# Performance work log

Hardware: AMD Instinct MI355X
Metric: run time of the kernel (lower is better)

The kernel has to match this reference:

```python
import jax, jax.numpy as jnp
import numpy as np

L, B, H, R = 128, 4, 768, 24
LN_EPS = 1e-5


def setup_inputs() -> dict:
    key = jax.random.key(0)
    ks = jax.random.split(key, 10)
    s = 1.0 / np.sqrt(H)
    return {
        "h_re": jax.random.normal(ks[0], (L, B, H), jnp.float32),
        "h_share": jax.random.normal(ks[1], (L, B, H), jnp.float32),
        "mask": jnp.ones((L, B), jnp.float32),
        # r: Linear(2H -> H)
        "r_w": jax.random.normal(ks[2], (H, 2 * H), jnp.float32) * s,
        "r_b": jnp.zeros((H,), jnp.float32),
        # hid2hid: Linear(3H -> H)
        "hid_w": jax.random.normal(ks[3], (H, 3 * H), jnp.float32) * s,
        "hid_b": jnp.zeros((H,), jnp.float32),
        # LayerNorm(H)
        "ln_g": jnp.ones((H,), jnp.float32),
        "ln_b": jnp.zeros((H,), jnp.float32),
        # hid2rel: Linear(H -> R)
        "rel_w": jax.random.normal(ks[4], (R, H), jnp.float32) * s,
        "rel_b": jnp.zeros((R,), jnp.float32),
    }


def reference(h_re, h_share, mask, r_w, r_b, hid_w, hid_b, ln_g, ln_b, rel_w, rel_b):
    # h_global = max_over_length( tanh( Linear([h_share; h_re]) ) )  -> [B, H]
    # Decompose concat-linear into two additive projections (same math).
    w_sh, w_re = r_w[:, :H], r_w[:, H:]
    g = jnp.tanh(jnp.einsum('lbh,kh->lbk', h_share, w_sh)
                 + jnp.einsum('lbh,kh->lbk', h_re, w_re) + r_b)
    g = jnp.max(g, axis=0)  # [B, H]

    # hid2hid(cat(r1, r2, g)) = h_re@W1^T (bcast over j) + h_re@W2^T (bcast over i) + g@W3^T + b
    w1, w2, w3 = hid_w[:, :H], hid_w[:, H:2 * H], hid_w[:, 2 * H:]
    p1 = jnp.einsum('lbh,kh->lbk', h_re, w1)        # [L, B, H] -> varies with i
    p2 = jnp.einsum('lbh,kh->lbk', h_re, w2)        # [L, B, H] -> varies with j
    pg = jnp.einsum('bh,kh->bk', g, w3) + hid_b     # [B, H]
    z = p1[:, None, :, :] + p2[None, :, :, :] + pg  # [L, L, B, H]

    # LayerNorm over last dim
    mu = jnp.mean(z, axis=-1, keepdims=True)
    var = jnp.mean(jnp.square(z - mu), axis=-1, keepdims=True)
    z = (z - mu) * jax.lax.rsqrt(var + LN_EPS) * ln_g + ln_b

    # ELU (dropout = identity in eval), then sigmoid(hid2rel)
    z = jax.nn.elu(z)
    re = jax.nn.sigmoid(jnp.einsum('ijbh,rh->ijbr', z, rel_w) + rel_b)  # [L, L, B, R]

    # pairwise mask: mask[i,b] * mask[j,b]
    m = mask[:, None, :] * mask[None, :, :]        # [L, L, B]
    return re * m[..., None]
```

## Files before the change

kernel.cpp:

```cpp
#include <hip/hip_runtime.h>
#include <hip/hip_bf16.h>
#include <math.h>

#define L 128
#define B 4
#define H 768
#define LN_EPS 1e-5f
#define XROWS 272
#define DSTRIDE 73984

typedef __attribute__((ext_vector_type(8))) short short8;
typedef __attribute__((ext_vector_type(4))) float f32x4;
typedef __attribute__((ext_vector_type(16))) float f32x16;

static __device__ __forceinline__ unsigned f2bfu(float f) {
    unsigned u = __float_as_uint(f);
    return (u + 0x7FFFu + ((u >> 16) & 1u)) >> 16;
}
static __device__ __forceinline__ uint2 pk4(float4 v) {
    uint2 o;
    o.x = f2bfu(v.x) | (f2bfu(v.y) << 16);
    o.y = f2bfu(v.z) | (f2bfu(v.w) << 16);
    return o;
}
static __device__ __forceinline__ unsigned short f2b(float f) {
    union { __hip_bfloat16 h; unsigned short u; } cv;
    cv.h = __float2bfloat16(f);
    return cv.u;
}
static __device__ __forceinline__ float4 unpk4(uint2 p) {
    return make_float4(__uint_as_float(p.x << 16),
                       __uint_as_float(p.x & 0xffff0000u),
                       __uint_as_float(p.y << 16),
                       __uint_as_float(p.y & 0xffff0000u));
}
static __device__ __forceinline__ unsigned fkey(float x) {
    unsigned u = __float_as_uint(x);
    return (u >> 31) ? ~u : (u | 0x80000000u);
}

__global__ __launch_bounds__(256) void kConv(const float* __restrict__ h_re,
                                             const float* __restrict__ h_share,
                                             const float* __restrict__ r_w,
                                             const float* __restrict__ hid_w,
                                             const float* __restrict__ rel_w,
                                             unsigned short* __restrict__ apack,
                                             unsigned short* __restrict__ wpackA,
                                             unsigned short* __restrict__ wpackB,
                                             unsigned short* __restrict__ rwb2,
                                             unsigned int* __restrict__ gmax) {
    int t = blockIdx.x * 256 + threadIdx.x;
    if (t >= 397056) return;
    if (t < 98304) {
        int m = t / 192, oct = t % 192, k = oct * 8;
        const float* src = (k < 768) ? (h_share + (size_t)m * 768 + k)
                                     : (h_re + (size_t)m * 768 + k - 768);
        float4 x = *(const float4*)src, y = *(const float4*)(src + 4);
        int mt = m >> 4, lr = m & 15, ks = k >> 5, lq = (k >> 3) & 3;
        uint2* dst = (uint2*)(apack + (((size_t)mt * 48 + ks) * 64 + lq * 16 + lr) * 8);
        dst[0] = pk4(x); dst[1] = pk4(y);
    } else if (t < 245760) {
        int t2 = t - 98304;
        int n = t2 / 192, oct = t2 % 192, k = oct * 8;
        const float* src = r_w + (size_t)n * 1536 + k;
        float4 x = *(const float4*)src, y = *(const float4*)(src + 4);
        int nt = n >> 4, lr = n & 15, ks = k >> 5, lq = (k >> 3) & 3;
        uint2* dst = (uint2*)(wpackA + (((size_t)nt * 48 + ks) * 64 + lq * 16 + lr) * 8);
        dst[0] = pk4(x); dst[1] = pk4(y);
    } else if (t < 393216) {
        int t3 = t - 245760;
        int n = t3 / 96, oct = t3 % 96, k = oct * 8;
        int half = (n >= 768) ? 1 : 0;
        const float* src = hid_w + (size_t)(n - half * 768) * 2304 + half * 768 + k;
        float4 x = *(const float4*)src, y = *(const float4*)(src + 4);
        int nt = n >> 4, lr = n & 15, ks = k >> 5, lq = (k >> 3) & 3;
        uint2* dst = (uint2*)(wpackB + (((size_t)nt * 24 + ks) * 64 + lq * 16 + lr) * 8);
        dst[0] = pk4(x); dst[1] = pk4(y);
    } else if (t < 396288) {
        int t4 = t - 393216;
        int s = t4 >> 6, l = t4 & 63;
        int row = l & 31;
        uint2 o0 = make_uint2(0u, 0u), o1 = o0;
        if (row < 24) {
            const float* src = rel_w + (size_t)row * 768 + s * 16 + (l >> 5) * 8;
            o0 = pk4(*(const float4*)src);
            o1 = pk4(*(const float4*)(src + 4));
        }
        uint2* dst = (uint2*)(rwb2 + (size_t)t4 * 8);
        dst[0] = o0; dst[1] = o1;
    } else {
        int t6 = t - 396288;
        gmax[t6] = 0u;
        gmax[768 + t6] = 0u;
        gmax[1536 + t6] = 0u;
        gmax[2304 + t6] = 0u;
    }
}

template<int KS>
static __device__ __forceinline__ void gemm_tile(const unsigned short* __restrict__ ap,
                                                 const unsigned short* __restrict__ wr,
                                                 f32x4 acc[2][2]) {
#pragma unroll 8
    for (int s = 0; s < KS; s++) {
        short8 a0 = *(const short8*)(ap + (size_t)s * 512);
        short8 a1 = *(const short8*)(ap + (size_t)(48 + s) * 512);
        short8 w0 = *(const short8*)(wr + (size_t)s * 512);
        short8 w1 = *(const short8*)(wr + (size_t)(KS + s) * 512);
        acc[0][0] = __builtin_amdgcn_mfma_f32_16x16x32_bf16(a0, w0, acc[0][0], 0, 0, 0);
        acc[0][1] = __builtin_amdgcn_mfma_f32_16x16x32_bf16(a0, w1, acc[0][1], 0, 0, 0);
        acc[1][0] = __builtin_amdgcn_mfma_f32_16x16x32_bf16(a1, w0, acc[1][0], 0, 0, 0);
        acc[1][1] = __builtin_amdgcn_mfma_f32_16x16x32_bf16(a1, w1, acc[1][1], 0, 0, 0);
    }
}

__global__ __launch_bounds__(64) void kGemm(const unsigned short* __restrict__ apack,
                                            const unsigned short* __restrict__ wpackA,
                                            const unsigned short* __restrict__ wpackB,
                                            unsigned int* __restrict__ gmax,
                                            unsigned short* __restrict__ xb16) {
    int id = blockIdx.x;
    int lane = threadIdx.x;
    int lq = lane >> 4, lr = lane & 15;
    f32x4 acc[2][2] = {{{0.f,0.f,0.f,0.f},{0.f,0.f,0.f,0.f}},
                       {{0.f,0.f,0.f,0.f},{0.f,0.f,0.f,0.f}}};
    if (id < 384) {
        int mt0 = (id / 24) * 2, nt0 = (id % 24) * 2;
        const unsigned short* ap = apack + (size_t)mt0 * 48 * 512 + lane * 8;
        const unsigned short* wr = wpackA + (size_t)nt0 * 48 * 512 + lane * 8;
        gemm_tile<48>(ap, wr, acc);
#pragma unroll
        for (int ni = 0; ni < 2; ni++)
#pragma unroll
            for (int q = 0; q < 4; q++) {
                float mx = fmaxf(acc[0][ni][q], acc[1][ni][q]);
                mx = fmaxf(mx, __shfl_xor(mx, 16, 64));
                mx = fmaxf(mx, __shfl_xor(mx, 32, 64));
                if (lq == 0) {
                    int n = (nt0 + ni) * 16 + lr;
                    atomicMax(&gmax[q * 768 + n], fkey(mx));
                }
            }
    } else {
        int id2 = id - 384;
        int mt0 = (id2 / 48) * 2, nt0 = (id2 % 48) * 2;
        const unsigned short* ap = apack + ((size_t)mt0 * 48 + 24) * 512 + lane * 8;
        const unsigned short* wr = wpackB + (size_t)nt0 * 24 * 512 + lane * 8;
        gemm_tile<24>(ap, wr, acc);
#pragma unroll
        for (int mi = 0; mi < 2; mi++)
#pragma unroll
            for (int ni = 0; ni < 2; ni++)
#pragma unroll
                for (int q = 0; q < 4; q++) {
                    int m = (mt0 + mi) * 16 + lq * 4 + q;
                    int n = (nt0 + ni) * 16 + lr;
                    int b = m & 3, l = m >> 2;
                    size_t row = (n < 768) ? (size_t)l : (size_t)(128 + l);
                    int col = (n < 768) ? n : n - 768;
                    xb16[((size_t)b * XROWS + row) * 768 + col] = f2b(acc[mi][ni][q]);
                }
    }
}

__global__ __launch_bounds__(256) void kPgPack(const unsigned int* __restrict__ gmax,
                                               const float* __restrict__ r_b,
                                               const float* __restrict__ hid_w,
                                               const float* __restrict__ hid_b,
                                               unsigned short* xb16,
                                               unsigned short* __restrict__ xpack) {
    int blk = blockIdx.x, tid = threadIdx.x;
    if (blk >= 48) {
        int t = (blk - 48) * 256 + tid;
        int b = t / 24576, rem = t % 24576;
        int r = rem / 96, k8 = rem % 96;
        const uint2* src = (const uint2*)(xb16 + ((size_t)b * XROWS + r) * 768 + k8 * 8);
        uint2 v0 = src[0], v1 = src[1];
        size_t dst = ((((size_t)(b * 17 + (r >> 4)) * 24 + (k8 >> 2)) * 64)
                      + (k8 & 3) * 16 + (r & 15)) * 8;
        uint2* d = (uint2*)(xpack + dst);
        d[0] = v0; d[1] = v1;
        return;
    }
    __shared__ float sg[768];
    __shared__ float sp[4][64];
    __shared__ float spg[64];
    int kt = blk % 12, b = blk / 12;
    for (int v = tid; v < 768; v += 256) {
        unsigned key = gmax[b * 768 + v];
        unsigned bits = (key & 0x80000000u) ? (key & 0x7FFFFFFFu) : ~key;
        sg[v] = tanhf(__uint_as_float(bits) + r_b[v]);
    }
    __syncthreads();
    int kk = tid & 63, hc = tid >> 6;
    int k = kt * 64 + kk;
    const float4* w4 = (const float4*)hid_w;
    const float4* g4 = (const float4*)sg;
    float acc = 0.f;
    for (int h = hc * 48; h < hc * 48 + 48; h++) {
        float4 gv = g4[h];
        float4 wv = w4[(size_t)k * 576 + 384 + h];
        acc += gv.x * wv.x + gv.y * wv.y + gv.z * wv.z + gv.w * wv.w;
    }
    sp[hc][kk] = acc;
    __syncthreads();
    if (hc == 0) {
        float pgv = sp[0][kk] + sp[1][kk] + sp[2][kk] + sp[3][kk] + hid_b[k];
        spg[kk] = pgv;
        xb16[((size_t)b * XROWS + 256) * 768 + k] = f2b(pgv);
    }
    __syncthreads();
    if (tid < 128) {
        int ksl = tid >> 6, lane = tid & 63;
        int ks = kt * 2 + ksl;
        int row16 = lane & 15;
        int kbase = ksl * 32 + (lane >> 4) * 8;
        unsigned short vals[8];
        if (row16 == 0) {
#pragma unroll
            for (int e = 0; e < 8; e++) vals[e] = f2b(spg[kbase + e]);
        } else if (row16 == 1) {
#pragma unroll
            for (int e = 0; e < 8; e++) vals[e] = 0x3F80;
        } else {
#pragma unroll
            for (int e = 0; e < 8; e++) vals[e] = 0;
        }
        uint2* d = (uint2*)(xpack + (((size_t)(b * 17 + 16) * 24 + ks) * 64 + lane) * 8);
        d[0] = *(uint2*)&vals[0];
        d[1] = *(uint2*)&vals[4];
    }
}

__global__ __launch_bounds__(64) void kGram(const unsigned short* __restrict__ xpack,
                                            float* __restrict__ D) {
    int t = blockIdx.x, b = blockIdx.y;
    int it, jt;
    if (t < 64)      { it = t >> 3;  jt = 8 + (t & 7); }
    else if (t < 80) { it = t - 64;  jt = t - 64; }
    else             { it = t - 80;  jt = 16; }
    int lane = threadIdx.x, lq = lane >> 4, lr = lane & 15;
    const unsigned short* ar = xpack + ((size_t)(b * 17 + it) * 24 * 64 + lane) * 8;
    const unsigned short* wr = xpack + ((size_t)(b * 17 + jt) * 24 * 64 + lane) * 8;
    f32x4 acc = {0.f, 0.f, 0.f, 0.f};
#pragma unroll 8
    for (int s = 0; s < 24; s++) {
        short8 a = *(const short8*)(ar + (size_t)s * 512);
        short8 w = *(const short8*)(wr + (size_t)s * 512);
        acc = __builtin_amdgcn_mfma_f32_16x16x32_bf16(a, w, acc, 0, 0, 0);
    }
    float* Db = D + (size_t)b * DSTRIDE;
#pragma unroll
    for (int q = 0; q < 4; q++)
        Db[(size_t)(it * 16 + lq * 4 + q) * XROWS + jt * 16 + lr] = acc[q];
}

__global__ __launch_bounds__(512, 6) void kC(const unsigned short* __restrict__ xb16,
                                             const float* __restrict__ ln_g,
                                             const float* __restrict__ ln_b,
                                             const unsigned short* __restrict__ rwb2,
                                             const float* __restrict__ rel_b,
                                             const float* __restrict__ D,
                                             const float* __restrict__ mask,
                                             float* __restrict__ out) {
    __shared__ __align__(16) unsigned char smem[49920];
    __shared__ float smu[32], srs[32];
    unsigned short (*zls)[780] = (unsigned short (*)[780])smem;
    int i = blockIdx.x, b = blockIdx.y, j0 = blockIdx.z * 32;
    int tid = threadIdx.x, lane = tid & 63, wave = tid >> 6;

    if (tid < 32) {
        const float* Db = D + (size_t)b * DSTRIDE;
        int vr = 128 + j0 + tid;
        float Su1 = Db[(size_t)i * XROWS + 257];
        float Su2 = Db[(size_t)i * XROWS + i];
        float up  = Db[(size_t)i * XROWS + 256];
        float Sp1 = Db[(size_t)256 * XROWS + 257];
        float Sp2 = Db[(size_t)256 * XROWS + 256];
        float Sv1 = Db[(size_t)vr * XROWS + 257];
        float Sv2 = Db[(size_t)vr * XROWS + vr];
        float Dij = Db[(size_t)i * XROWS + vr];
        float cvj = Db[(size_t)vr * XROWS + 256];
        float s1 = Su1 + Sp1 + Sv1;
        float s2 = Su2 + Sp2 + Sv2 + 2.f * (Dij + up + cvj);
        float mu = s1 * (1.f / 768.f);
        smu[tid] = mu;
        srs[tid] = rsqrtf(s2 * (1.f / 768.f) - mu * mu + LN_EPS);
    }
    const uint2* ur = (const uint2*)(xb16 + ((size_t)b * XROWS + i) * 768);
    const uint2* pr = (const uint2*)(xb16 + ((size_t)b * XROWS + 256) * 768);
    const float4* lg4 = (const float4*)ln_g;
    const float4* lb4 = (const float4*)ln_b;
    float4 t1[3], gg[3], bb[3];
#pragma unroll
    for (int s = 0; s < 3; s++) {
        int c = lane + 64 * s;
        float4 x = unpk4(ur[c]), y = unpk4(pr[c]);
        t1[s] = make_float4(x.x + y.x, x.y + y.y, x.z + y.z, x.w + y.w);
        gg[s] = lg4[c];
        bb[s] = lb4[c];
    }
    __syncthreads();

#pragma unroll
    for (int jj = 0; jj < 4; jj++) {
        int j = wave * 4 + jj;
        float mu = smu[j], rs = srs[j];
        const uint2* vr2 = (const uint2*)(xb16 + ((size_t)b * XROWS + 128 + j0 + j) * 768);
        uint2* zrow = (uint2*)&zls[j][0];
#pragma unroll
        for (int s = 0; s < 3; s++) {
            int c = lane + 64 * s;
            float4 vv = unpk4(vr2[c]);
            float A0 = rs * gg[s].x, A1 = rs * gg[s].y, A2 = rs * gg[s].z, A3 = rs * gg[s].w;
            float C0 = fmaf(-mu, A0, bb[s].x), C1 = fmaf(-mu, A1, bb[s].y);
            float C2 = fmaf(-mu, A2, bb[s].z), C3 = fmaf(-mu, A3, bb[s].w);
            float z0 = fmaf(t1[s].x + vv.x, A0, C0);
            float z1 = fmaf(t1[s].y + vv.y, A1, C1);
            float z2 = fmaf(t1[s].z + vv.z, A2, C2);
            float z3 = fmaf(t1[s].w + vv.w, A3, C3);
            z0 = fmaxf(z0, __expf(fminf(z0, 0.f)) - 1.f);
            z1 = fmaxf(z1, __expf(fminf(z1, 0.f)) - 1.f);
            z2 = fmaxf(z2, __expf(fminf(z2, 0.f)) - 1.f);
            z3 = fmaxf(z3, __expf(fminf(z3, 0.f)) - 1.f);
            uint2 o;
            o.x = (unsigned)f2b(z0) | ((unsigned)f2b(z1) << 16);
            o.y = (unsigned)f2b(z2) | ((unsigned)f2b(z3) << 16);
            zrow[c] = o;
        }
    }
    __syncthreads();

    int arow = lane & 31, ahi = lane >> 5;
    f32x16 acc = {0.f,0.f,0.f,0.f, 0.f,0.f,0.f,0.f, 0.f,0.f,0.f,0.f, 0.f,0.f,0.f,0.f};
    const unsigned short* bptr = rwb2 + ((size_t)(wave * 6) * 64 + lane) * 8;
#pragma unroll
    for (int st = 0; st < 6; st++) {
        int s = wave * 6 + st;
        short8 a  = *(const short8*)&zls[arow][s * 16 + ahi * 8];
        short8 bf = *(const short8*)(bptr + (size_t)st * 512);
        acc = __builtin_amdgcn_mfma_f32_32x32x16_bf16(a, bf, acc, 0, 0, 0);
    }
    __syncthreads();
    float* pf = (float*)smem;
#pragma unroll
    for (int r = 0; r < 16; r++) {
        int row = (r & 3) + 8 * (r >> 2) + 4 * ahi;
        pf[wave * 1024 + row * 32 + arow] = acc[r];
    }
    __syncthreads();

#pragma unroll
    for (int e0 = 0; e0 < 2; e0++) {
        int e = tid + e0 * 512;
        int row = e >> 5, col = e & 31;
        if (col < 24) {
            float v = 0.f;
#pragma unroll
            for (int w = 0; w < 8; w++) v += pf[w * 1024 + e];
            int jgl = j0 + row;
            float mval = mask[i * 4 + b] * mask[jgl * 4 + b];
            out[((size_t)(i * 128 + jgl) * 4 + b) * 24 + col] =
                mval / (1.f + __expf(-(v + rel_b[col])));
        }
    }
}

extern "C" void kernel_launch(void* const* d_in, const int* in_sizes, int n_in,
                              void* d_out, int out_size, void* d_ws, size_t ws_size,
                              hipStream_t stream) {
    const float* h_re    = (const float*)d_in[0];
    const float* h_share = (const float*)d_in[1];
    const float* mask    = (const float*)d_in[2];
    const float* r_w     = (const float*)d_in[3];
    const float* r_b     = (const float*)d_in[4];
    const float* hid_w   = (const float*)d_in[5];
    const float* hid_b   = (const float*)d_in[6];
    const float* ln_g    = (const float*)d_in[7];
    const float* ln_b    = (const float*)d_in[8];
    const float* rel_w   = (const float*)d_in[9];
    const float* rel_b   = (const float*)d_in[10];
    float* out = (float*)d_out;

    float* ws = (float*)d_ws;
    unsigned short* apack  = (unsigned short*)(ws);
    unsigned short* wpackA = (unsigned short*)(ws + 393216);
    unsigned short* wpackB = (unsigned short*)(ws + 983040);
    unsigned short* xb16   = (unsigned short*)(ws + 1572864);
    float*          D      = ws + 1990656;
    unsigned int*   gmax   = (unsigned int*)(ws + 2286592);
    unsigned short* rwb2   = (unsigned short*)(ws + 2289664);
    unsigned short* xpack  = (unsigned short*)(ws);

    kConv<<<1552, 256, 0, stream>>>(h_re, h_share, r_w, hid_w, rel_w,
                                    apack, wpackA, wpackB, rwb2, gmax);
    kGemm<<<1152, 64, 0, stream>>>(apack, wpackA, wpackB, gmax, xb16);
    kPgPack<<<432, 256, 0, stream>>>(gmax, r_b, hid_w, hid_b, xb16, xpack);
    kGram<<<dim3(97, 4), 64, 0, stream>>>(xpack, D);
    kC<<<dim3(L, B, 4), 512, 0, stream>>>(xb16, ln_g, ln_b, rwb2, rel_b,
                                          D, mask, out);
}
```

Measured before the change: 73.46 us.

## Split GEMM K-loop across four waves with LDS reduction

The projection GEMM kernel now runs four wavefronts per block, each handling a quarter of the K dimension. Partial accumulators are reduced through shared memory before the max/atomic or store epilogue. The aim is to shorten each block's serial MFMA chain and expose more parallelism and memory-level concurrency. The cost is extra LDS traffic, a block barrier, and three idle waves during the epilogue.

```diff
diff --git a/kernel.cpp b/kernel.cpp
--- a/kernel.cpp
+++ b/kernel.cpp
@@ -97,16 +97,18 @@
     }
 }
 
-template<int KS>
-static __device__ __forceinline__ void gemm_tile(const unsigned short* __restrict__ ap,
-                                                 const unsigned short* __restrict__ wr,
-                                                 f32x4 acc[2][2]) {
-#pragma unroll 8
-    for (int s = 0; s < KS; s++) {
-        short8 a0 = *(const short8*)(ap + (size_t)s * 512);
-        short8 a1 = *(const short8*)(ap + (size_t)(48 + s) * 512);
-        short8 w0 = *(const short8*)(wr + (size_t)s * 512);
-        short8 w1 = *(const short8*)(wr + (size_t)(KS + s) * 512);
+template<int KSW>
+static __device__ __forceinline__ void gemm_steps(const unsigned short* __restrict__ a0p,
+                                                  const unsigned short* __restrict__ a1p,
+                                                  const unsigned short* __restrict__ w0p,
+                                                  const unsigned short* __restrict__ w1p,
+                                                  f32x4 acc[2][2]) {
+#pragma unroll
+    for (int s = 0; s < KSW; s++) {
+        short8 a0 = *(const short8*)(a0p + (size_t)s * 512);
+        short8 a1 = *(const short8*)(a1p + (size_t)s * 512);
+        short8 w0 = *(const short8*)(w0p + (size_t)s * 512);
+        short8 w1 = *(const short8*)(w1p + (size_t)s * 512);
         acc[0][0] = __builtin_amdgcn_mfma_f32_16x16x32_bf16(a0, w0, acc[0][0], 0, 0, 0);
         acc[0][1] = __builtin_amdgcn_mfma_f32_16x16x32_bf16(a0, w1, acc[0][1], 0, 0, 0);
         acc[1][0] = __builtin_amdgcn_mfma_f32_16x16x32_bf16(a1, w0, acc[1][0], 0, 0, 0);
@@ -114,26 +116,59 @@
     }
 }
 
-__global__ __launch_bounds__(64) void kGemm(const unsigned short* __restrict__ apack,
-                                            const unsigned short* __restrict__ wpackA,
-                                            const unsigned short* __restrict__ wpackB,
-                                            unsigned int* __restrict__ gmax,
-                                            unsigned short* __restrict__ xb16) {
+__global__ __launch_bounds__(256) void kGemm(const unsigned short* __restrict__ apack,
+                                             const unsigned short* __restrict__ wpackA,
+                                             const unsigned short* __restrict__ wpackB,
+                                             unsigned int* __restrict__ gmax,
+                                             unsigned short* __restrict__ xb16) {
+    __shared__ float red[4][4][64][4];
     int id = blockIdx.x;
-    int lane = threadIdx.x;
+    int tid = threadIdx.x, lane = tid & 63, wv = tid >> 6;
     int lq = lane >> 4, lr = lane & 15;
+    bool isA = id < 384;
     f32x4 acc[2][2] = {{{0.f,0.f,0.f,0.f},{0.f,0.f,0.f,0.f}},
                        {{0.f,0.f,0.f,0.f},{0.f,0.f,0.f,0.f}}};
-    if (id < 384) {
-        int mt0 = (id / 24) * 2, nt0 = (id % 24) * 2;
-        const unsigned short* ap = apack + (size_t)mt0 * 48 * 512 + lane * 8;
-        const unsigned short* wr = wpackA + (size_t)nt0 * 48 * 512 + lane * 8;
-        gemm_tile<48>(ap, wr, acc);
+    int mt0, nt0;
+    if (isA) {
+        mt0 = (id / 24) * 2; nt0 = (id % 24) * 2;
+        const unsigned short* a0p = apack + ((size_t)mt0 * 48 + wv * 12) * 512 + lane * 8;
+        const unsigned short* w0p = wpackA + ((size_t)nt0 * 48 + wv * 12) * 512 + lane * 8;
+        gemm_steps<12>(a0p, a0p + 48 * 512, w0p, w0p + 48 * 512, acc);
+    } else {
+        int id2 = id - 384;
+        mt0 = (id2 / 48) * 2; nt0 = (id2 % 48) * 2;
+        const unsigned short* a0p = apack + ((size_t)mt0 * 48 + 24 + wv * 6) * 512 + lane * 8;
+        const unsigned short* w0p = wpackB + ((size_t)nt0 * 24 + wv * 6) * 512 + lane * 8;
+        gemm_steps<6>(a0p, a0p + 48 * 512, w0p, w0p + 24 * 512, acc);
+    }
+#pragma unroll
+    for (int mi = 0; mi < 2; mi++)
 #pragma unroll
         for (int ni = 0; ni < 2; ni++)
+            *(f32x4*)&red[wv][mi * 2 + ni][lane][0] = acc[mi][ni];
+    __syncthreads();
+    if (wv != 0) return;
+
+    f32x4 s2[2][2];
+#pragma unroll
+    for (int mi = 0; mi < 2; mi++)
+#pragma unroll
+        for (int ni = 0; ni < 2; ni++) {
+            f32x4 v = *(f32x4*)&red[0][mi * 2 + ni][lane][0];
+#pragma unroll
+            for (int w = 1; w < 4; w++) {
+                f32x4 u = *(f32x4*)&red[w][mi * 2 + ni][lane][0];
+                v[0] += u[0]; v[1] += u[1]; v[2] += u[2]; v[3] += u[3];
+            }
+            s2[mi][ni] = v;
+        }
+
+    if (isA) {
+#pragma unroll
+        for (int ni = 0; ni < 2; ni++)
 #pragma unroll
             for (int q = 0; q < 4; q++) {
-                float mx = fmaxf(acc[0][ni][q], acc[1][ni][q]);
+                float mx = fmaxf(s2[0][ni][q], s2[1][ni][q]);
                 mx = fmaxf(mx, __shfl_xor(mx, 16, 64));
                 mx = fmaxf(mx, __shfl_xor(mx, 32, 64));
                 if (lq == 0) {
@@ -142,11 +177,6 @@
                 }
             }
     } else {
-        int id2 = id - 384;
-        int mt0 = (id2 / 48) * 2, nt0 = (id2 % 48) * 2;
-        const unsigned short* ap = apack + ((size_t)mt0 * 48 + 24) * 512 + lane * 8;
-        const unsigned short* wr = wpackB + (size_t)nt0 * 24 * 512 + lane * 8;
-        gemm_tile<24>(ap, wr, acc);
 #pragma unroll
         for (int mi = 0; mi < 2; mi++)
 #pragma unroll
@@ -158,7 +188,7 @@
                     int b = m & 3, l = m >> 2;
                     size_t row = (n < 768) ? (size_t)l : (size_t)(128 + l);
                     int col = (n < 768) ? n : n - 768;
-                    xb16[((size_t)b * XROWS + row) * 768 + col] = f2b(acc[mi][ni][q]);
+                    xb16[((size_t)b * XROWS + row) * 768 + col] = f2b(s2[mi][ni][q]);
                 }
     }
 }
@@ -394,7 +424,7 @@
 
     kConv<<<1552, 256, 0, stream>>>(h_re, h_share, r_w, hid_w, rel_w,
                                     apack, wpackA, wpackB, rwb2, gmax);
-    kGemm<<<1152, 64, 0, stream>>>(apack, wpackA, wpackB, gmax, xb16);
+    kGemm<<<1152, 256, 0, stream>>>(apack, wpackA, wpackB, gmax, xb16);
     kPgPack<<<432, 256, 0, stream>>>(gmax, r_b, hid_w, hid_b, xb16, xpack);
     kGram<<<dim3(97, 4), 64, 0, stream>>>(xpack, D);
     kC<<<dim3(L, B, 4), 512, 0, stream>>>(xb16, ln_g, ln_b, rwb2, rel_b,
```

Result: faster. 65.89 us (-10.3%).
